# Performance work log

Hardware: AMD Instinct MI355X
Metric: run time of the kernel (lower is better)

Reference implementation:

```python
import jax, jax.numpy as jnp
import numpy as np

HID = 1024
NH = 16
DH = HID // NH  # 64


def _heads(x):
    # [B, S, H] -> [B, nH, S, dh]
    B, S, _ = x.shape
    return x.reshape(B, S, NH, DH).transpose(0, 2, 1, 3)


def setup_inputs() -> dict:
    key = jax.random.key(0)
    ks = jax.random.split(key, 16)
    inp = {
        "word_hidden_states": jax.random.normal(ks[0], (2, 2048, HID), jnp.float32),
        "entity_hidden_states": jax.random.normal(ks[1], (2, 256, HID), jnp.float32),
    }
    scale = 1.0 / np.sqrt(HID)
    names = ["Wq", "Wk", "Wv", "Ww2e", "We2w", "We2e"]
    for i, n in enumerate(names):
        inp[n] = jax.random.normal(ks[2 + i], (HID, HID), jnp.float32) * scale
        inp["b" + n[1:]] = jnp.zeros((HID,), jnp.float32)
    return inp


def reference(word_hidden_states, entity_hidden_states,
              Wq, bq, Wk, bk, Wv, bv,
              Ww2e, bw2e, We2w, be2w, We2e, be2e):
    word, ent = word_hidden_states, entity_hidden_states
    B, Sw, _ = word.shape
    Se = ent.shape[1]
    hs = jnp.concatenate([word, ent], axis=1)  # [B, Sw+Se, H]

    # four query types, heads: [B, nH, S*, dh]
    q_w2w = _heads(word @ Wq + bq)
    q_w2e = _heads(word @ Ww2e + bw2e)
    q_e2w = _heads(ent @ We2w + be2w)
    q_e2e = _heads(ent @ We2e + be2e)

    k = _heads(hs @ Wk + bk)
    v = _heads(hs @ Wv + bv)
    k_w, k_e = k[:, :, :Sw, :], k[:, :, Sw:, :]

    # block scores
    s_w2w = jnp.einsum("bhqd,bhkd->bhqk", q_w2w, k_w)  # [B,nH,Sw,Sw]
    s_w2e = jnp.einsum("bhqd,bhkd->bhqk", q_w2e, k_e)  # [B,nH,Sw,Se]
    s_e2w = jnp.einsum("bhqd,bhkd->bhqk", q_e2w, k_w)  # [B,nH,Se,Sw]
    s_e2e = jnp.einsum("bhqd,bhkd->bhqk", q_e2e, k_e)  # [B,nH,Se,Se]

    word_scores = jnp.concatenate([s_w2w, s_w2e], axis=3)
    ent_scores = jnp.concatenate([s_e2w, s_e2e], axis=3)
    scores = jnp.concatenate([word_scores, ent_scores], axis=2)  # [B,nH,S,S]
    scores = scores / np.sqrt(DH)

    probs = jax.nn.softmax(scores, axis=-1)  # dropout is identity in eval
    ctx = jnp.einsum("bhqk,bhkd->bhqd", probs, v)  # [B,nH,S,dh]
    ctx = ctx.transpose(0, 2, 1, 3).reshape(B, Sw + Se, HID)
    return ctx[:, :Sw, :], ctx[:, Sw:, :]
```

## Files before the change

kernel.cpp:

```cpp
#include <hip/hip_runtime.h>
#include <hip/hip_bf16.h>

typedef __attribute__((ext_vector_type(8))) short short8;
typedef __attribute__((ext_vector_type(4))) float f32x4;
typedef __attribute__((ext_vector_type(16))) float f32x16;
typedef __attribute__((ext_vector_type(4))) unsigned short u16x4;
typedef __attribute__((ext_vector_type(8))) unsigned short u16x8;
typedef __attribute__((ext_vector_type(4))) unsigned int u32x4;

__device__ __forceinline__ unsigned short f2b(float f) {
  __hip_bfloat16 h = __float2bfloat16(f);
  return __builtin_bit_cast(unsigned short, h);
}

__device__ __forceinline__ void gload_lds16(const void* g, void* l) {
  __builtin_amdgcn_global_load_lds(
      (const __attribute__((address_space(1))) unsigned int*)g,
      (__attribute__((address_space(3))) unsigned int*)l, 16, 0, 0);
}

__device__ __forceinline__ f32x16 mfma32(short8 a, short8 b, f32x16 c) {
  return __builtin_amdgcn_mfma_f32_32x32x16_bf16(a, b, c, 0, 0, 0);
}

__device__ __forceinline__ unsigned int cvtpk(float a, float b) {
  unsigned int r;
  asm("v_cvt_pk_bf16_f32 %0, %1, %2" : "=v"(r) : "v"(a), "v"(b));
  return r;
}

struct PrepassParams {
  const float* sw;
  const float* se;
  unsigned short* dw;
  unsigned short* de;
  const float* w[6];
  unsigned short* wt[6];
};

__global__ __launch_bounds__(256) void prepass(PrepassParams p) {
  const int bx = blockIdx.x;
  const int tid = threadIdx.x;
  if (bx < 2304) {
    int i = bx * 256 + tid;
    const float* s;
    unsigned short* d;
    int j;
    if (i < 524288) {
      s = p.sw; d = p.dw; j = i;
    } else {
      s = p.se; d = p.de; j = i - 524288;
      if (j >= 65536) return;
    }
    const f32x4* sp = (const f32x4*)s;
    f32x4 a = sp[2 * j];
    f32x4 b = sp[2 * j + 1];
    u16x8 o;
    o[0] = f2b(a[0]); o[1] = f2b(a[1]); o[2] = f2b(a[2]); o[3] = f2b(a[3]);
    o[4] = f2b(b[0]); o[5] = f2b(b[1]); o[6] = f2b(b[2]); o[7] = f2b(b[3]);
    ((u16x8*)d)[j] = o;
  } else {
    __shared__ float t[32][33];
    const int idx = bx - 2304;
    const int z = idx >> 10;
    const int rem = idx & 1023;
    const int bxx = rem & 31;
    const int byy = rem >> 5;
    const float* W = p.w[z];
    unsigned short* Wt = p.wt[z];
    const int tx = tid & 31, ty = tid >> 5;
#pragma unroll
    for (int i = 0; i < 4; ++i)
      t[ty + 8 * i][tx] = W[(byy * 32 + ty + 8 * i) * 1024 + bxx * 32 + tx];
    __syncthreads();
#pragma unroll
    for (int i = 0; i < 4; ++i)
      Wt[(bxx * 32 + ty + 8 * i) * 1024 + byy * 32 + tx] = f2b(t[tx][ty + 8 * i]);
  }
}

struct GemmJob {
  const unsigned short* Wt;
  const float* bias;
  unsigned short* out;
  int S;
  int s_off;
  int sshift;
  int trans;
  float scale;
};
struct Gemm2Params {
  const unsigned short* Aw;
  const unsigned short* Ae;
  GemmJob job[8];
};

__global__ __launch_bounds__(256) void gemm_qkv(Gemm2Params p) {
  __shared__ unsigned short smem[16384];
  unsigned short* As = smem;
  unsigned short* Bs = smem + 8192;
  const int tid = threadIdx.x;
  const int w = tid >> 6, lane = tid & 63;
  const int c = lane & 15, g = lane >> 4;
  const int z = blockIdx.z;
  const int y = blockIdx.y;
  const bool isword = y < 32;
  const GemmJob j = p.job[isword ? z : z + 4];
  const unsigned short* A = isword ? p.Aw : p.Ae;
  const long arow0 = (long)(isword ? y : y - 32) * 128;
  const unsigned short* B = j.Wt;
  const long brow0 = (long)blockIdx.x * 128;

  f32x4 acc[4][4] = {};

  for (int kt = 0; kt < 16; ++kt) {
    __syncthreads();
#pragma unroll
    for (int i = 0; i < 4; ++i) {
      int ch = i * 256 + tid;
      int row = ch >> 3;
      int k8 = ((ch & 7) ^ (row & 7)) << 3;
      const unsigned short* ga = A + (arow0 + row) * 1024 + kt * 64 + k8;
      const unsigned short* gb = B + (brow0 + row) * 1024 + kt * 64 + k8;
      gload_lds16(ga, As + (i * 256 + w * 64) * 8);
      gload_lds16(gb, Bs + (i * 256 + w * 64) * 8);
    }
    __syncthreads();
#pragma unroll
    for (int kf = 0; kf < 2; ++kf) {
      short8 av[4], bv[4];
#pragma unroll
      for (int mf = 0; mf < 4; ++mf) {
        int row = (w >> 1) * 64 + mf * 16 + c;
        int byte = (row * 128 + (kf * 32 + g * 8) * 2) ^ ((row & 7) << 4);
        av[mf] = *(const short8*)((const char*)As + byte);
      }
#pragma unroll
      for (int nf = 0; nf < 4; ++nf) {
        int row = (w & 1) * 64 + nf * 16 + c;
        int byte = (row * 128 + (kf * 32 + g * 8) * 2) ^ ((row & 7) << 4);
        bv[nf] = *(const short8*)((const char*)Bs + byte);
      }
      __builtin_amdgcn_s_setprio(1);
#pragma unroll
      for (int mf = 0; mf < 4; ++mf)
#pragma unroll
        for (int nf = 0; nf < 4; ++nf)
          acc[mf][nf] = __builtin_amdgcn_mfma_f32_16x16x32_bf16(av[mf], bv[nf],
                                                                acc[mf][nf], 0, 0, 0);
      __builtin_amdgcn_s_setprio(0);
    }
  }

  float biasv[4];
#pragma unroll
  for (int nf = 0; nf < 4; ++nf) {
    int n = (int)brow0 + (w & 1) * 64 + nf * 16 + c;
    biasv[nf] = j.bias[n];
  }
  const int smask = (1 << j.sshift) - 1;
  __syncthreads();

  if (j.trans) {
#pragma unroll
    for (int mf = 0; mf < 4; ++mf) {
      int m0 = (w >> 1) * 64 + mf * 16 + g * 4;
#pragma unroll
      for (int nf = 0; nf < 4; ++nf) {
        int n = (w & 1) * 64 + nf * 16 + c;
        u16x4 pv;
#pragma unroll
        for (int r = 0; r < 4; ++r)
          pv[r] = f2b((acc[mf][nf][r] + biasv[nf]) * j.scale);
        int byte = (n * 256 + m0 * 2) ^ ((n & 7) << 4);
        *(u16x4*)((char*)smem + byte) = pv;
      }
    }
    __syncthreads();
#pragma unroll
    for (int i = 0; i < 8; ++i) {
      int ch = i * 256 + tid;
      int nr = ch >> 4, sl = ch & 15;
      int byte = (nr * 256 + sl * 16) ^ ((nr & 7) << 4);
      u16x8 v = *(const u16x8*)((const char*)smem + byte);
      int n = (int)brow0 + nr;
      int hh = n >> 6, dd = n & 63;
      int m = (int)arow0 + sl * 8;
      int b_ = m >> j.sshift;
      int s = (m & smask) + j.s_off;
      *(u16x8*)(j.out + (((long)b_ * 16 + hh) * 64 + dd) * 2304 + s) = v;
    }
  } else {
#pragma unroll
    for (int mf = 0; mf < 4; ++mf) {
#pragma unroll
      for (int r = 0; r < 4; ++r) {
        int m = (w >> 1) * 64 + mf * 16 + g * 4 + r;
#pragma unroll
        for (int nf = 0; nf < 4; ++nf) {
          int n = (w & 1) * 64 + nf * 16 + c;
          unsigned short hv = f2b((acc[mf][nf][r] + biasv[nf]) * j.scale);
          int byte = (m * 256 + n * 2) ^ ((m & 7) << 4);
          *(unsigned short*)((char*)smem + byte) = hv;
        }
      }
    }
    __syncthreads();
#pragma unroll
    for (int i = 0; i < 8; ++i) {
      int ch = i * 256 + tid;
      int mr = ch >> 4, sl = ch & 15;
      int byte = (mr * 256 + sl * 16) ^ ((mr & 7) << 4);
      u16x8 v = *(const u16x8*)((const char*)smem + byte);
      int m = (int)arow0 + mr;
      int b_ = m >> j.sshift;
      int s = (m & smask) + j.s_off;
      int n = (int)brow0 + sl * 8;
      int hh = n >> 6, dd = n & 63;
      *(u16x8*)(j.out + (((long)b_ * 16 + hh) * j.S + s) * 64 + dd) = v;
    }
  }
}

__global__ __launch_bounds__(256) void attn_kernel(
    const unsigned short* __restrict__ qw2w, const unsigned short* __restrict__ qw2e,
    const unsigned short* __restrict__ qe2w, const unsigned short* __restrict__ qe2e,
    const unsigned short* __restrict__ Kg, const unsigned short* __restrict__ Vtg,
    float* __restrict__ po0, float* __restrict__ po1, float* __restrict__ lbuf) {
  __shared__ unsigned short smem[16384];

  const int tid = threadIdx.x;
  const int w = tid >> 6, lane = tid & 63;
  const int l31 = lane & 31, hf = lane >> 5;

  const int flat = blockIdx.x;
  const int work = (flat & 7) * 144 + (flat >> 3);
  const int part = work & 1;
  const int tile = (work % 36) >> 1;
  const int hb = work / 36;
  const int head = hb & 15, b = hb >> 4;

  const bool isw = tile < 16;
  const int Sq = isw ? 2048 : 256;
  const int q0 = (isw ? tile : tile - 16) * 128 + w * 32;
  const int bh = b * 16 + head;
  const unsigned short* Qa =
      (isw ? qw2w : qe2w) + ((long)bh * Sq + q0 + l31) * 64 + hf * 8;
  const unsigned short* Qb =
      (isw ? qw2e : qe2e) + ((long)bh * Sq + q0 + l31) * 64 + hf * 8;
  const unsigned short* Kb = Kg + (long)bh * 2304 * 64;
  const unsigned short* Vtb = Vtg + (long)bh * 64 * 2304;

  short8 qcur[4];
#pragma unroll
  for (int kf = 0; kf < 4; ++kf) qcur[kf] = *(const short8*)(Qa + kf * 16);

  f32x16 o[2] = {};
  float lrun = 0.f;

  auto stage = [&](int t, int bufi) {
    const unsigned short* Kt = Kb + t * 4096;
    unsigned short* Klp = smem + bufi * 4096;
    unsigned short* Vlp = smem + 8192 + bufi * 4096;
#pragma unroll
    for (int i = 0; i < 2; ++i) {
      int ch = i * 256 + tid;
      int row = ch >> 3, c8 = ch & 7;
      int col = (c8 ^ (row & 7)) << 3;
      gload_lds16(Kt + row * 64 + col, Klp + (i * 256 + (tid & 192)) * 8);
      gload_lds16(Vtb + row * 2304 + t * 64 + col, Vlp + (i * 256 + (tid & 192)) * 8);
    }
  };

  const int t0 = part * 18, t1 = t0 + 18;
  stage(t0, 0);
  int cur = 0;

  for (int t = t0; t < t1; ++t) {
    if (t == 32) {
#pragma unroll
      for (int kf = 0; kf < 4; ++kf) qcur[kf] = *(const short8*)(Qb + kf * 16);
    }
    if (t + 1 < t1) {
      stage(t + 1, cur ^ 1);
      asm volatile("s_waitcnt vmcnt(4)" ::: "memory");
    } else {
      asm volatile("s_waitcnt vmcnt(0)" ::: "memory");
    }
    __builtin_amdgcn_sched_barrier(0);
    __builtin_amdgcn_s_barrier();

    const char* Kbase = (const char*)(smem + cur * 4096);
    const char* Vbase = (const char*)(smem + 8192 + cur * 4096);

    f32x16 st[2] = {};
#pragma unroll
    for (int kg = 0; kg < 2; ++kg) {
      int row = kg * 32 + l31;
      int rb = (row * 128) | (hf * 16);
      int sw = (row & 7) << 4;
      short8 kfr[4];
#pragma unroll
      for (int kf = 0; kf < 4; ++kf)
        kfr[kf] = *(const short8*)(Kbase + ((rb + kf * 32) ^ sw));
      __builtin_amdgcn_s_setprio(1);
#pragma unroll
      for (int kf = 0; kf < 4; ++kf) st[kg] = mfma32(kfr[kf], qcur[kf], st[kg]);
      __builtin_amdgcn_s_setprio(0);
    }

    float s0 = 0.f, s1 = 0.f, s2 = 0.f, s3 = 0.f;
#pragma unroll
    for (int kg = 0; kg < 2; ++kg) {
#pragma unroll
      for (int r = 0; r < 16; r += 4) {
        float p0 = __builtin_amdgcn_exp2f(st[kg][r + 0]);
        float p1 = __builtin_amdgcn_exp2f(st[kg][r + 1]);
        float p2 = __builtin_amdgcn_exp2f(st[kg][r + 2]);
        float p3 = __builtin_amdgcn_exp2f(st[kg][r + 3]);
        st[kg][r + 0] = p0; st[kg][r + 1] = p1;
        st[kg][r + 2] = p2; st[kg][r + 3] = p3;
        s0 += p0; s1 += p1; s2 += p2; s3 += p3;
      }
    }
    lrun += (s0 + s1) + (s2 + s3);

#pragma unroll
    for (int kg = 0; kg < 2; ++kg)
#pragma unroll
      for (int hs = 0; hs < 2; ++hs) {
        const int rbase = hs * 8;
        unsigned int a0 = cvtpk(st[kg][rbase + 0], st[kg][rbase + 1]);
        unsigned int a1 = cvtpk(st[kg][rbase + 2], st[kg][rbase + 3]);
        unsigned int b0 = cvtpk(st[kg][rbase + 4], st[kg][rbase + 5]);
        unsigned int b1 = cvtpk(st[kg][rbase + 6], st[kg][rbase + 7]);
        asm("v_permlane32_swap_b32 %0, %1" : "+v"(a0), "+v"(b0));
        asm("v_permlane32_swap_b32 %0, %1" : "+v"(a1), "+v"(b1));
        u32x4 pw;
        pw[0] = a0; pw[1] = a1; pw[2] = b0; pw[3] = b1;
        short8 pf = __builtin_bit_cast(short8, pw);
        const int ks = kg * 2 + hs;
        short8 vf0, vf1;
        {
          int vrow = l31;
          int byte = ((vrow * 128) | (ks * 32 + hf * 16)) ^ ((vrow & 7) << 4);
          vf0 = *(const short8*)(Vbase + byte);
          vrow = 32 + l31;
          byte = ((vrow * 128) | (ks * 32 + hf * 16)) ^ ((vrow & 7) << 4);
          vf1 = *(const short8*)(Vbase + byte);
        }
        __builtin_amdgcn_s_setprio(1);
        o[0] = mfma32(vf0, pf, o[0]);
        o[1] = mfma32(vf1, pf, o[1]);
        __builtin_amdgcn_s_setprio(0);
      }

    asm volatile("s_waitcnt lgkmcnt(0)" ::: "memory");
    __builtin_amdgcn_sched_barrier(0);
    __builtin_amdgcn_s_barrier();
    cur ^= 1;
  }

  float ltot = lrun + __shfl_xor(lrun, 32);

  const int sgb = (isw ? 0 : 2048) + q0;
  if (hf == 0) lbuf[(long)part * 73728 + bh * 2304 + sgb + l31] = ltot;

  float* E = (float*)smem + w * 2048;
#pragma unroll
  for (int mf = 0; mf < 2; ++mf)
#pragma unroll
    for (int rg = 0; rg < 4; ++rg) {
      int d0 = mf * 32 + rg * 8 + hf * 4;
      f32x4 v;
      v[0] = o[mf][rg * 4 + 0];
      v[1] = o[mf][rg * 4 + 1];
      v[2] = o[mf][rg * 4 + 2];
      v[3] = o[mf][rg * 4 + 3];
      *(f32x4*)(E + l31 * 64 + (d0 ^ ((l31 & 7) << 2))) = v;
    }

  float* po = part ? po1 : po0;
  float* ob = isw ? po + (((long)b * 2048 + q0) * 1024 + head * 64)
                  : po + (long)2 * 2048 * 1024 +
                        (((long)b * 256 + q0) * 1024 + head * 64);
#pragma unroll
  for (int i = 0; i < 8; ++i) {
    int qr = (lane >> 4) + i * 4;
    int dc = (lane & 15) * 4;
    f32x4 v = *(const f32x4*)(E + qr * 64 + (dc ^ ((qr & 7) << 2)));
    *(f32x4*)(ob + (long)qr * 1024 + dc) = v;
  }
}

__global__ __launch_bounds__(256) void attn_merge(const float* __restrict__ po0,
                                                  const float* __restrict__ po1,
                                                  const float* __restrict__ lbuf,
                                                  float* __restrict__ out) {
  long i = ((long)blockIdx.x * 256 + threadIdx.x) * 4;
  if (i >= 4718592) return;
  int bh, sg;
  if (i < 4194304) {
    int b = (int)(i >> 21), s = (int)((i >> 10) & 2047), h = (int)((i >> 6) & 15);
    bh = b * 16 + h;
    sg = s;
  } else {
    long j = i - 4194304;
    int b = (int)(j >> 18), s = (int)((j >> 10) & 255), h = (int)((j >> 6) & 15);
    bh = b * 16 + h;
    sg = 2048 + s;
  }
  float l0 = lbuf[bh * 2304 + sg];
  float l1 = lbuf[73728 + bh * 2304 + sg];
  f32x4 a = *(const f32x4*)(po0 + i);
  f32x4 c = *(const f32x4*)(po1 + i);
  float inv = 1.f / (l0 + l1);
  f32x4 r = (a + c) * inv;
  *(f32x4*)(out + i) = r;
}

extern "C" void kernel_launch(void* const* d_in, const int* in_sizes, int n_in,
                              void* d_out, int out_size, void* d_ws, size_t ws_size,
                              hipStream_t stream) {
  (void)in_sizes; (void)n_in; (void)out_size; (void)ws_size;
  const float* word = (const float*)d_in[0];
  const float* ent = (const float*)d_in[1];

  char* ws = (char*)d_ws;
  size_t off = 0;
  auto alloc = [&](size_t bytes) {
    void* p = ws + off;
    off += (bytes + 255) & ~(size_t)255;
    return p;
  };
  unsigned short* Xw = (unsigned short*)alloc(4096ull * 1024 * 2);
  unsigned short* Xe = (unsigned short*)alloc(512ull * 1024 * 2);
  unsigned short* Wt[6];
  for (int i = 0; i < 6; ++i) Wt[i] = (unsigned short*)alloc(1024ull * 1024 * 2);
  unsigned short* qw2w = (unsigned short*)alloc(2ull * 16 * 2048 * 64 * 2);
  unsigned short* qw2e = (unsigned short*)alloc(2ull * 16 * 2048 * 64 * 2);
  unsigned short* qe2w = (unsigned short*)alloc(2ull * 16 * 256 * 64 * 2);
  unsigned short* qe2e = (unsigned short*)alloc(2ull * 16 * 256 * 64 * 2);
  unsigned short* Kbuf = (unsigned short*)alloc(2ull * 16 * 2304 * 64 * 2);
  unsigned short* Vtbuf = (unsigned short*)alloc(2ull * 16 * 64 * 2304 * 2);
  float* po1 = (float*)alloc(4718592ull * 4);
  float* lbuf = (float*)alloc(2ull * 73728 * 4);
  float* po0 = (float*)ws;

  PrepassParams pp;
  pp.sw = word;
  pp.se = ent;
  pp.dw = Xw;
  pp.de = Xe;
  pp.w[0] = (const float*)d_in[2];
  pp.w[1] = (const float*)d_in[4];
  pp.w[2] = (const float*)d_in[6];
  pp.w[3] = (const float*)d_in[8];
  pp.w[4] = (const float*)d_in[10];
  pp.w[5] = (const float*)d_in[12];
  for (int i = 0; i < 6; ++i) pp.wt[i] = Wt[i];
  prepass<<<8448, 256, 0, stream>>>(pp);

  const float* bq = (const float*)d_in[3];
  const float* bk = (const float*)d_in[5];
  const float* bv = (const float*)d_in[7];
  const float* bw2e = (const float*)d_in[9];
  const float* be2w = (const float*)d_in[11];
  const float* be2e = (const float*)d_in[13];
  const float qs = 0.125f * 1.44269504f;

  Gemm2Params gp;
  gp.Aw = Xw;
  gp.Ae = Xe;
  gp.job[0] = {Wt[0], bq, qw2w, 2048, 0, 11, 0, qs};
  gp.job[1] = {Wt[3], bw2e, qw2e, 2048, 0, 11, 0, qs};
  gp.job[2] = {Wt[1], bk, Kbuf, 2304, 0, 11, 0, 1.f};
  gp.job[3] = {Wt[2], bv, Vtbuf, 2304, 0, 11, 1, 1.f};
  gp.job[4] = {Wt[4], be2w, qe2w, 256, 0, 8, 0, qs};
  gp.job[5] = {Wt[5], be2e, qe2e, 256, 0, 8, 0, qs};
  gp.job[6] = {Wt[1], bk, Kbuf, 2304, 2048, 8, 0, 1.f};
  gp.job[7] = {Wt[2], bv, Vtbuf, 2304, 2048, 8, 1, 1.f};
  gemm_qkv<<<dim3(8, 36, 4), 256, 0, stream>>>(gp);

  attn_kernel<<<1152, 256, 0, stream>>>(qw2w, qw2e, qe2w, qe2e, Kbuf, Vtbuf,
                                        po0, po1, lbuf);
  attn_merge<<<4608, 256, 0, stream>>>(po0, po1, lbuf, (float*)d_out);
}
```

Before: 148.1 us.

## Merge split-KV halves inside one 512-thread block, drop merge kernel

Each attention block now runs both key-range halves as two groups of four waves with separate LDS staging. The partial outputs and row sums are combined in shared memory and normalised before the final store. This removes the fp32 partial-output round trip through global memory and the separate merge launch. V staging is also changed from double-buffered to single-buffered, loaded after the barrier, which may expose V load latency and needs more LDS per block, lowering occupancy.

Measured after the change: 151.0 us. No clear change (+2.0%).

```diff
diff --git a/kernel.cpp b/kernel.cpp
--- a/kernel.cpp
+++ b/kernel.cpp
@@ -222,27 +222,28 @@
   }
 }
 
-__global__ __launch_bounds__(256) void attn_kernel(
+__global__ __launch_bounds__(512) void attn_kernel(
     const unsigned short* __restrict__ qw2w, const unsigned short* __restrict__ qw2e,
     const unsigned short* __restrict__ qe2w, const unsigned short* __restrict__ qe2e,
     const unsigned short* __restrict__ Kg, const unsigned short* __restrict__ Vtg,
-    float* __restrict__ po0, float* __restrict__ po1, float* __restrict__ lbuf) {
-  __shared__ unsigned short smem[16384];
+    float* __restrict__ out) {
+  __shared__ unsigned short smem[24576];
 
   const int tid = threadIdx.x;
   const int w = tid >> 6, lane = tid & 63;
   const int l31 = lane & 31, hf = lane >> 5;
+  const int part = w >> 2, wq = w & 3;
+  const int tpid = tid & 255;
 
   const int flat = blockIdx.x;
-  const int work = (flat & 7) * 144 + (flat >> 3);
-  const int part = work & 1;
-  const int tile = (work % 36) >> 1;
-  const int hb = work / 36;
+  const int work = (flat & 7) * 72 + (flat >> 3);
+  const int tile = work % 18;
+  const int hb = work / 18;
   const int head = hb & 15, b = hb >> 4;
 
   const bool isw = tile < 16;
   const int Sq = isw ? 2048 : 256;
-  const int q0 = (isw ? tile : tile - 16) * 128 + w * 32;
+  const int q0 = (isw ? tile : tile - 16) * 128 + wq * 32;
   const int bh = b * 16 + head;
   const unsigned short* Qa =
       (isw ? qw2w : qe2w) + ((long)bh * Sq + q0 + l31) * 64 + hf * 8;
@@ -258,40 +259,52 @@
   f32x16 o[2] = {};
   float lrun = 0.f;
 
-  auto stage = [&](int t, int bufi) {
-    const unsigned short* Kt = Kb + t * 4096;
-    unsigned short* Klp = smem + bufi * 4096;
-    unsigned short* Vlp = smem + 8192 + bufi * 4096;
+  unsigned short* partbase = smem + part * 12288;
+  const int keyb = part * 1152;
+
+  auto stage_K = [&](int t, int bufi) {
+    unsigned short* Klp = partbase + bufi * 4096;
 #pragma unroll
     for (int i = 0; i < 2; ++i) {
-      int ch = i * 256 + tid;
+      int ch = i * 256 + tpid;
       int row = ch >> 3, c8 = ch & 7;
       int col = (c8 ^ (row & 7)) << 3;
-      gload_lds16(Kt + row * 64 + col, Klp + (i * 256 + (tid & 192)) * 8);
-      gload_lds16(Vtb + row * 2304 + t * 64 + col, Vlp + (i * 256 + (tid & 192)) * 8);
+      gload_lds16(Kb + (keyb + t * 64 + row) * 64 + col,
+                  Klp + (i * 256 + (tpid & 192)) * 8);
     }
   };
-
-  const int t0 = part * 18, t1 = t0 + 18;
-  stage(t0, 0);
+  auto stage_V = [&](int t) {
+    unsigned short* Vlp = partbase + 8192;
+#pragma unroll
+    for (int i = 0; i < 2; ++i) {
+      int ch = i * 256 + tpid;
+      int row = ch >> 3, c8 = ch & 7;
+      int col = (c8 ^ (row & 7)) << 3;
+      gload_lds16(Vtb + row * 2304 + keyb + t * 64 + col,
+                  Vlp + (i * 256 + (tpid & 192)) * 8);
+    }
+  };
+
+  stage_K(0, 0);
+  stage_V(0);
   int cur = 0;
 
-  for (int t = t0; t < t1; ++t) {
-    if (t == 32) {
+  for (int t = 0; t < 18; ++t) {
+    if (part == 1 && t == 14) {
 #pragma unroll
       for (int kf = 0; kf < 4; ++kf) qcur[kf] = *(const short8*)(Qb + kf * 16);
     }
-    if (t + 1 < t1) {
-      stage(t + 1, cur ^ 1);
-      asm volatile("s_waitcnt vmcnt(4)" ::: "memory");
+    if (t < 17) {
+      stage_K(t + 1, cur ^ 1);
+      asm volatile("s_waitcnt vmcnt(2)" ::: "memory");
     } else {
       asm volatile("s_waitcnt vmcnt(0)" ::: "memory");
     }
     __builtin_amdgcn_sched_barrier(0);
     __builtin_amdgcn_s_barrier();
 
-    const char* Kbase = (const char*)(smem + cur * 4096);
-    const char* Vbase = (const char*)(smem + 8192 + cur * 4096);
+    const char* Kbase = (const char*)(partbase + cur * 4096);
+    const char* Vbase = (const char*)(partbase + 8192);
 
     f32x16 st[2] = {};
 #pragma unroll
@@ -358,65 +371,64 @@
     asm volatile("s_waitcnt lgkmcnt(0)" ::: "memory");
     __builtin_amdgcn_sched_barrier(0);
     __builtin_amdgcn_s_barrier();
+    if (t < 17) stage_V(t + 1);
     cur ^= 1;
   }
 
-  float ltot = lrun + __shfl_xor(lrun, 32);
-
-  const int sgb = (isw ? 0 : 2048) + q0;
-  if (hf == 0) lbuf[(long)part * 73728 + bh * 2304 + sgb + l31] = ltot;
-
-  float* E = (float*)smem + w * 2048;
-#pragma unroll
-  for (int mf = 0; mf < 2; ++mf)
-#pragma unroll
-    for (int rg = 0; rg < 4; ++rg) {
-      int d0 = mf * 32 + rg * 8 + hf * 4;
-      f32x4 v;
-      v[0] = o[mf][rg * 4 + 0];
-      v[1] = o[mf][rg * 4 + 1];
-      v[2] = o[mf][rg * 4 + 2];
-      v[3] = o[mf][rg * 4 + 3];
-      *(f32x4*)(E + l31 * 64 + (d0 ^ ((l31 & 7) << 2))) = v;
-    }
-
-  float* po = part ? po1 : po0;
-  float* ob = isw ? po + (((long)b * 2048 + q0) * 1024 + head * 64)
-                  : po + (long)2 * 2048 * 1024 +
-                        (((long)b * 256 + q0) * 1024 + head * 64);
-#pragma unroll
-  for (int i = 0; i < 8; ++i) {
-    int qr = (lane >> 4) + i * 4;
-    int dc = (lane & 15) * 4;
-    f32x4 v = *(const f32x4*)(E + qr * 64 + (dc ^ ((qr & 7) << 2)));
-    *(f32x4*)(ob + (long)qr * 1024 + dc) = v;
-  }
-}
-
-__global__ __launch_bounds__(256) void attn_merge(const float* __restrict__ po0,
-                                                  const float* __restrict__ po1,
-                                                  const float* __restrict__ lbuf,
-                                                  float* __restrict__ out) {
-  long i = ((long)blockIdx.x * 256 + threadIdx.x) * 4;
-  if (i >= 4718592) return;
-  int bh, sg;
-  if (i < 4194304) {
-    int b = (int)(i >> 21), s = (int)((i >> 10) & 2047), h = (int)((i >> 6) & 15);
-    bh = b * 16 + h;
-    sg = s;
+  float lt = lrun + __shfl_xor(lrun, 32);
+  float* Lf = (float*)(smem + 16384);
+
+  if (part == 0) {
+    if (lane < 32) Lf[wq * 32 + lane] = lt;
+#pragma unroll
+    for (int mf = 0; mf < 2; ++mf)
+#pragma unroll
+      for (int rg = 0; rg < 4; ++rg) {
+        int d4 = mf * 8 + rg * 2 + hf;
+        f32x4 v;
+        v[0] = o[mf][rg * 4 + 0];
+        v[1] = o[mf][rg * 4 + 1];
+        v[2] = o[mf][rg * 4 + 2];
+        v[3] = o[mf][rg * 4 + 3];
+        *(f32x4*)((char*)smem + wq * 8192 + l31 * 256 + ((d4 ^ (l31 & 7)) << 4)) = v;
+      }
   } else {
-    long j = i - 4194304;
-    int b = (int)(j >> 18), s = (int)((j >> 10) & 255), h = (int)((j >> 6) & 15);
-    bh = b * 16 + h;
-    sg = 2048 + s;
-  }
-  float l0 = lbuf[bh * 2304 + sg];
-  float l1 = lbuf[73728 + bh * 2304 + sg];
-  f32x4 a = *(const f32x4*)(po0 + i);
-  f32x4 c = *(const f32x4*)(po1 + i);
-  float inv = 1.f / (l0 + l1);
-  f32x4 r = (a + c) * inv;
-  *(f32x4*)(out + i) = r;
+    if (lane < 32) Lf[128 + wq * 32 + lane] = lt;
+  }
+  __syncthreads();
+
+  if (part == 1) {
+#pragma unroll
+    for (int mf = 0; mf < 2; ++mf)
+#pragma unroll
+      for (int rg = 0; rg < 4; ++rg) {
+        int d4 = mf * 8 + rg * 2 + hf;
+        char* ptr =
+            (char*)smem + wq * 8192 + l31 * 256 + ((d4 ^ (l31 & 7)) << 4);
+        f32x4 pv = *(f32x4*)ptr;
+        pv[0] += o[mf][rg * 4 + 0];
+        pv[1] += o[mf][rg * 4 + 1];
+        pv[2] += o[mf][rg * 4 + 2];
+        pv[3] += o[mf][rg * 4 + 3];
+        *(f32x4*)ptr = pv;
+      }
+  }
+  __syncthreads();
+
+  const int qblk0 = (isw ? tile : tile - 16) * 128;
+  float* ob = isw ? out + (((long)b * 2048 + qblk0) * 1024 + head * 64)
+                  : out + 4194304 + (((long)b * 256 + qblk0) * 1024 + head * 64);
+#pragma unroll
+  for (int i = 0; i < 4; ++i) {
+    int idx = i * 512 + tid;
+    int q = idx >> 4, ch = idx & 15;
+    int ql = q & 31;
+    f32x4 v = *(const f32x4*)((const char*)smem + (q >> 5) * 8192 + ql * 256 +
+                              ((ch ^ (ql & 7)) << 4));
+    float inv = 1.f / (Lf[q] + Lf[128 + q]);
+    v *= inv;
+    *(f32x4*)(ob + (long)q * 1024 + ch * 4) = v;
+  }
 }
 
 extern "C" void kernel_launch(void* const* d_in, const int* in_sizes, int n_in,
@@ -443,9 +455,6 @@
   unsigned short* qe2e = (unsigned short*)alloc(2ull * 16 * 256 * 64 * 2);
   unsigned short* Kbuf = (unsigned short*)alloc(2ull * 16 * 2304 * 64 * 2);
   unsigned short* Vtbuf = (unsigned short*)alloc(2ull * 16 * 64 * 2304 * 2);
-  float* po1 = (float*)alloc(4718592ull * 4);
-  float* lbuf = (float*)alloc(2ull * 73728 * 4);
-  float* po0 = (float*)ws;
 
   PrepassParams pp;
   pp.sw = word;
@@ -482,7 +491,6 @@
   gp.job[7] = {Wt[2], bv, Vtbuf, 2304, 2048, 8, 1, 1.f};
   gemm_qkv<<<dim3(8, 36, 4), 256, 0, stream>>>(gp);
 
-  attn_kernel<<<1152, 256, 0, stream>>>(qw2w, qw2e, qe2w, qe2e, Kbuf, Vtbuf,
-                                        po0, po1, lbuf);
-  attn_merge<<<4608, 256, 0, stream>>>(po0, po1, lbuf, (float*)d_out);
-}
+  attn_kernel<<<576, 512, 0, stream>>>(qw2w, qw2e, qe2w, qe2e, Kbuf, Vtbuf,
+                                       (float*)d_out);
+}
```
